# Performance work log

Hardware: AMD Instinct MI355X
Metric: run time of the kernel (lower is better)

Reference implementation:

```python
import jax, jax.numpy as jnp
import numpy as np

ALPHA = 1000.0


def setup_inputs() -> dict:
    key = jax.random.key(0)
    ks = jax.random.split(key, 5)
    B, D_in, K = 8192, 2048, 256  # K = n_clusters = embed_dim (square cluster_reps)
    x = jax.random.normal(ks[0], (B, D_in), dtype=jnp.float32)
    W_enc = jax.random.normal(ks[1], (D_in, K), dtype=jnp.float32) * (1.0 / np.sqrt(D_in))
    b_enc = jnp.zeros((K,), dtype=jnp.float32)
    W_dec = jax.random.normal(ks[2], (K, D_in), dtype=jnp.float32) * (1.0 / np.sqrt(K))
    b_dec = jnp.zeros((D_in,), dtype=jnp.float32)
    cluster_reps = jax.random.normal(ks[3], (K, K), dtype=jnp.float32)
    return {"x": x, "W_enc": W_enc, "b_enc": b_enc, "W_dec": W_dec,
            "b_dec": b_dec, "cluster_reps": cluster_reps}


def reference(x, W_enc, b_enc, W_dec, b_dec, cluster_reps):
    # Autoencoder (linear MLP stand-in for the injected module)
    emb = x @ W_enc + b_enc                    # [B, K]
    reconstruction = emb @ W_dec + b_dec       # [B, D_in]

    # Squared Euclidean distance to each cluster rep, in GEMM form: [B, K]
    # dist[b, k] = ||emb_b||^2 - 2 emb_b . c_k + ||c_k||^2
    dist = (jnp.sum(emb * emb, axis=1, keepdims=True)
            - 2.0 * (emb @ cluster_reps.T)
            + jnp.sum(cluster_reps * cluster_reps, axis=1)[None, :])

    stack_dist = dist.T                        # [K, B] (matches torch.stack over clusters)
    min_dist = jnp.min(stack_dist, axis=0)     # [B]
    stack_exp = jnp.exp(-ALPHA * (stack_dist - min_dist[None, :]))  # stable softmin
    softmax = stack_exp / jnp.sum(stack_exp, axis=0, keepdims=True)
    weighted_dist = stack_dist * softmax       # [K, B]
    return weighted_dist, reconstruction
```

## Files before the change

### kernel.cpp

```cpp
#include <hip/hip_runtime.h>

#define ALPHA_F 1000.0f

typedef _Float16 half8 __attribute__((ext_vector_type(8)));
typedef float floatx4 __attribute__((ext_vector_type(4)));

__device__ __forceinline__ void gload_lds16(const void* g, void* l) {
    __builtin_amdgcn_global_load_lds(
        (const __attribute__((address_space(1))) unsigned int*)g,
        (__attribute__((address_space(3))) unsigned int*)l, 16, 0, 0);
}

__global__ __launch_bounds__(256) void prep(
    const float* __restrict__ W_enc, const float* __restrict__ W_dec,
    const float* __restrict__ creps,
    _Float16* __restrict__ Wh, _Float16* __restrict__ Wl,
    _Float16* __restrict__ Wdh,
    _Float16* __restrict__ Ch, _Float16* __restrict__ Cl,
    float* __restrict__ cnorm)
{
    const int bid = blockIdx.x;
    if (bid < 256) {
        const int q = bid * 256 + threadIdx.x;
        const int n = q & 255, k8 = q >> 8;
        const int k = k8 * 8;
        half8 h, l;
        #pragma unroll
        for (int i = 0; i < 8; ++i) {
            const float v = W_enc[(size_t)(k + i) * 256 + n] * 256.0f;
            const _Float16 hi = (_Float16)v;
            h[i] = hi;
            l[i] = (_Float16)(v - (float)hi);
        }
        const int kc = k >> 5, nt = n >> 4;
        const int lane = (n & 15) | ((k8 & 3) << 4);
        const size_t idx = (size_t)((kc * 16 + nt) * 64 + lane) * 8;
        *(half8*)(Wh + idx) = h;
        *(half8*)(Wl + idx) = l;
    } else if (bid < 512) {
        const int q = (bid - 256) * 256 + threadIdx.x;
        const int n = q & 2047, k8 = q >> 11;
        const int k = k8 * 8;
        half8 h;
        #pragma unroll
        for (int i = 0; i < 8; ++i) h[i] = (_Float16)W_dec[(size_t)(k + i) * 2048 + n];
        const int kc = k8 >> 2, nt = n >> 4;
        const int lane = (n & 15) | ((k8 & 3) << 4);
        *(half8*)(Wdh + (size_t)((kc * 128 + nt) * 64 + lane) * 8) = h;
    } else if (bid < 544) {
        const int q = (bid - 512) * 256 + threadIdx.x;
        const int n = q & 255, j8 = q >> 8;
        const int j = j8 * 8;
        half8 h, l;
        #pragma unroll
        for (int i = 0; i < 8; ++i) {
            const float v = creps[(size_t)n * 256 + j + i];
            const _Float16 hi = (_Float16)v;
            h[i] = hi;
            l[i] = (_Float16)((v - (float)hi) * 2048.0f);
        }
        const int jc = j >> 5, nt = n >> 4;
        const int lane = (n & 15) | ((j8 & 3) << 4);
        const size_t idx = (size_t)((jc * 16 + nt) * 64 + lane) * 8;
        *(half8*)(Ch + idx) = h;
        *(half8*)(Cl + idx) = l;
    } else {
        const int wid = threadIdx.x >> 6, lane = threadIdx.x & 63;
        const int row = (bid - 544) * 4 + wid;
        const float4 v = *(const float4*)(creps + (size_t)row * 256 + lane * 4);
        float s = v.x * v.x + v.y * v.y + v.z * v.z + v.w * v.w;
        #pragma unroll
        for (int off = 32; off >= 1; off >>= 1) s += __shfl_xor(s, off, 64);
        if (lane == 0) cnorm[row] = s;
    }
}

__global__ __launch_bounds__(256) void emb_gemm(
    const float* __restrict__ x, const _Float16* __restrict__ Wh,
    const _Float16* __restrict__ Wl, float* __restrict__ P)
{
    __shared__ _Float16 Ah[2][4 * 64 * 8], Al[2][4 * 64 * 8];
    __shared__ _Float16 Bh[2][16 * 64 * 8], Bl[2][16 * 64 * 8];
    const int t = threadIdx.x, lane = t & 63, w = t >> 6;
    const int kk = blockIdx.x;
    const int mb = blockIdx.y;
    const int m0 = mb * 64;

    const int am = t >> 2, q = t & 3;
    const int aoff = (((am >> 4) * 64) + ((am & 15) | (q << 4))) * 8;
    const float* xP = x + (size_t)(m0 + am) * 2048 + kk * 512 + q * 8;

    floatx4 acc[4][4] = {};

    {
        const float4 v0 = *(const float4*)(xP);
        const float4 v1 = *(const float4*)(xP + 4);
        const int kc = kk * 16;
        const _Float16* bh_src = Wh + (size_t)kc * 16 * 512;
        const _Float16* bl_src = Wl + (size_t)kc * 16 * 512;
        #pragma unroll
        for (int i = 0; i < 4; ++i) {
            const int c = w * 4 + i;
            gload_lds16(bh_src + (size_t)c * 512 + lane * 8, &Bh[0][c * 512]);
            gload_lds16(bl_src + (size_t)c * 512 + lane * 8, &Bl[0][c * 512]);
        }
        const float vv[8] = {v0.x, v0.y, v0.z, v0.w, v1.x, v1.y, v1.z, v1.w};
        half8 h8, l8;
        #pragma unroll
        for (int i = 0; i < 8; ++i) {
            const _Float16 hi = (_Float16)vv[i];
            h8[i] = hi;
            l8[i] = (_Float16)(vv[i] - (float)hi);
        }
        *(half8*)(&Ah[0][aoff]) = h8;
        *(half8*)(&Al[0][aoff]) = l8;
        __syncthreads();
    }

    for (int it = 0; it < 16; ++it) {
        const int buf = it & 1;

        float4 n0, n1;
        if (it < 15) {
            n0 = *(const float4*)(xP + (it + 1) * 32);
            n1 = *(const float4*)(xP + (it + 1) * 32 + 4);
            const int kc = kk * 16 + it + 1;
            const _Float16* bh_src = Wh + (size_t)kc * 16 * 512;
            const _Float16* bl_src = Wl + (size_t)kc * 16 * 512;
            #pragma unroll
            for (int i = 0; i < 4; ++i) {
                const int c = w * 4 + i;
                gload_lds16(bh_src + (size_t)c * 512 + lane * 8, &Bh[buf ^ 1][c * 512]);
                gload_lds16(bl_src + (size_t)c * 512 + lane * 8, &Bl[buf ^ 1][c * 512]);
            }
        }

        half8 ah[4], al[4], bh[4], bl[4];
        #pragma unroll
        for (int s = 0; s < 4; ++s) {
            ah[s] = *(const half8*)(&Ah[buf][(s * 64 + lane) * 8]);
            al[s] = *(const half8*)(&Al[buf][(s * 64 + lane) * 8]);
        }
        #pragma unroll
        for (int ni = 0; ni < 4; ++ni) {
            bh[ni] = *(const half8*)(&Bh[buf][((w * 4 + ni) * 64 + lane) * 8]);
            bl[ni] = *(const half8*)(&Bl[buf][((w * 4 + ni) * 64 + lane) * 8]);
        }
        #pragma unroll
        for (int mi = 0; mi < 4; ++mi) {
            #pragma unroll
            for (int ni = 0; ni < 4; ++ni) {
                acc[mi][ni] = __builtin_amdgcn_mfma_f32_16x16x32_f16(ah[mi], bl[ni], acc[mi][ni], 0, 0, 0);
                acc[mi][ni] = __builtin_amdgcn_mfma_f32_16x16x32_f16(al[mi], bh[ni], acc[mi][ni], 0, 0, 0);
                acc[mi][ni] = __builtin_amdgcn_mfma_f32_16x16x32_f16(ah[mi], bh[ni], acc[mi][ni], 0, 0, 0);
            }
        }

        if (it < 15) {
            const float vv[8] = {n0.x, n0.y, n0.z, n0.w, n1.x, n1.y, n1.z, n1.w};
            half8 h8, l8;
            #pragma unroll
            for (int i = 0; i < 8; ++i) {
                const _Float16 hi = (_Float16)vv[i];
                h8[i] = hi;
                l8[i] = (_Float16)(vv[i] - (float)hi);
            }
            *(half8*)(&Ah[buf ^ 1][aoff]) = h8;
            *(half8*)(&Al[buf ^ 1][aoff]) = l8;
            __syncthreads();
        }
    }

    float* Pk = P + (size_t)kk * 2097152;
    #pragma unroll
    for (int mi = 0; mi < 4; ++mi) {
        #pragma unroll
        for (int ni = 0; ni < 4; ++ni) {
            const int col = w * 64 + ni * 16 + (lane & 15);
            const int rowBase = m0 + mi * 16 + (lane >> 4) * 4;
            #pragma unroll
            for (int r = 0; r < 4; ++r)
                Pk[(size_t)(rowBase + r) * 256 + col] = acc[mi][ni][r];
        }
    }
}

__global__ __launch_bounds__(256) void finalize(
    const float* __restrict__ P, const float* __restrict__ b_enc,
    _Float16* __restrict__ ehg, float* __restrict__ embf,
    float* __restrict__ enorm)
{
    const int t = threadIdx.x;
    const int b0 = blockIdx.x * 32;
    const int row = t >> 3, c8 = t & 7;
    const int grow = b0 + row;

    const float* p0 = P + (size_t)grow * 256 + c8 * 32;
    float4 v[8];
    #pragma unroll
    for (int i = 0; i < 8; ++i) v[i] = *(const float4*)(p0 + i * 4);
    #pragma unroll
    for (int kk = 1; kk < 4; ++kk) {
        const float* pk = p0 + (size_t)kk * 2097152;
        #pragma unroll
        for (int i = 0; i < 8; ++i) {
            const float4 a = *(const float4*)(pk + i * 4);
            v[i].x += a.x; v[i].y += a.y; v[i].z += a.z; v[i].w += a.w;
        }
    }
    const float inv = 1.0f / 256.0f;
    float e[32];
    float ssq = 0.0f;
    #pragma unroll
    for (int i = 0; i < 8; ++i) {
        const float4 b = *(const float4*)(b_enc + c8 * 32 + i * 4);
        e[i * 4 + 0] = v[i].x * inv + b.x;
        e[i * 4 + 1] = v[i].y * inv + b.y;
        e[i * 4 + 2] = v[i].z * inv + b.z;
        e[i * 4 + 3] = v[i].w * inv + b.w;
        ssq += e[i * 4 + 0] * e[i * 4 + 0];
        ssq += e[i * 4 + 1] * e[i * 4 + 1];
        ssq += e[i * 4 + 2] * e[i * 4 + 2];
        ssq += e[i * 4 + 3] * e[i * 4 + 3];
    }
    #pragma unroll
    for (int i = 0; i < 8; ++i) {
        float4 s4;
        s4.x = e[i * 4 + 0]; s4.y = e[i * 4 + 1];
        s4.z = e[i * 4 + 2]; s4.w = e[i * 4 + 3];
        *(float4*)(embf + (size_t)grow * 256 + c8 * 32 + i * 4) = s4;
    }
    #pragma unroll
    for (int oo = 0; oo < 4; ++oo) {
        const int q = c8 * 4 + oo;
        half8 h;
        #pragma unroll
        for (int i = 0; i < 8; ++i) h[i] = (_Float16)e[oo * 8 + i];
        const size_t idx = (size_t)(((grow >> 4) * 8 + (q >> 2)) * 64
                                    + ((grow & 15) | ((q & 3) << 4))) * 8;
        *(half8*)(ehg + idx) = h;
    }
    ssq += __shfl_xor(ssq, 1, 64);
    ssq += __shfl_xor(ssq, 2, 64);
    ssq += __shfl_xor(ssq, 4, 64);
    if (c8 == 0) enorm[grow] = ssq;
}

__global__ __launch_bounds__(256) void dist16(
    const float* __restrict__ embf, const _Float16* __restrict__ ch,
    const _Float16* __restrict__ cl, const float* __restrict__ enorm,
    const float* __restrict__ cnorm, float* __restrict__ out)
{
    __shared__ float D[16 * 257];
    __shared__ float MINV[16], SUMV[16];
    const int t = threadIdx.x, lane = t & 63, w = t >> 6;
    const int b0 = blockIdx.x * 16;
    const int arow16 = lane & 15, aoct = lane >> 4;

    floatx4 acc[4] = {}, accX[4] = {};
    for (int kc = 0; kc < 8; ++kc) {
        const float* fp = embf + (size_t)(b0 + arow16) * 256 + kc * 32 + aoct * 8;
        const float4 u0 = *(const float4*)(fp);
        const float4 u1 = *(const float4*)(fp + 4);
        const float vv[8] = {u0.x, u0.y, u0.z, u0.w, u1.x, u1.y, u1.z, u1.w};
        half8 ah, al;
        #pragma unroll
        for (int j = 0; j < 8; ++j) {
            const _Float16 hi = (_Float16)vv[j];
            ah[j] = hi;
            al[j] = (_Float16)((vv[j] - (float)hi) * 2048.0f);
        }
        #pragma unroll
        for (int ni = 0; ni < 4; ++ni) {
            const size_t bb = (size_t)((kc * 16 + (w * 4 + ni)) * 64 + lane) * 8;
            const half8 bh = *(const half8*)(ch + bb);
            const half8 bl = *(const half8*)(cl + bb);
            acc[ni]  = __builtin_amdgcn_mfma_f32_16x16x32_f16(ah, bh, acc[ni], 0, 0, 0);
            accX[ni] = __builtin_amdgcn_mfma_f32_16x16x32_f16(ah, bl, accX[ni], 0, 0, 0);
            accX[ni] = __builtin_amdgcn_mfma_f32_16x16x32_f16(al, bh, accX[ni], 0, 0, 0);
        }
    }

    const float invs = 1.0f / 2048.0f;
    #pragma unroll
    for (int ni = 0; ni < 4; ++ni) {
        const int k = w * 64 + ni * 16 + (lane & 15);
        const float cn = cnorm[k];
        #pragma unroll
        for (int r = 0; r < 4; ++r) {
            const int rl = (lane >> 4) * 4 + r;
            const float S = acc[ni][r] + accX[ni][r] * invs;
            D[rl * 257 + k] = enorm[b0 + rl] - 2.0f * S + cn;
        }
    }
    __syncthreads();

    #pragma unroll
    for (int rr = 0; rr < 4; ++rr) {
        const int r = w * 4 + rr;
        const float d0 = D[r * 257 + lane +   0];
        const float d1 = D[r * 257 + lane +  64];
        const float d2 = D[r * 257 + lane + 128];
        const float d3 = D[r * 257 + lane + 192];
        float mn = fminf(fminf(d0, d1), fminf(d2, d3));
        #pragma unroll
        for (int off = 32; off >= 1; off >>= 1) mn = fminf(mn, __shfl_xor(mn, off, 64));
        float s = expf(-ALPHA_F * (d0 - mn)) + expf(-ALPHA_F * (d1 - mn))
                + expf(-ALPHA_F * (d2 - mn)) + expf(-ALPHA_F * (d3 - mn));
        #pragma unroll
        for (int off = 32; off >= 1; off >>= 1) s += __shfl_xor(s, off, 64);
        if (lane == 0) { MINV[r] = mn; SUMV[r] = s; }
    }
    __syncthreads();

    const int b = t & 15, kg = t >> 4;
    const float mn = MINV[b], sv = SUMV[b];
    #pragma unroll
    for (int kk = 0; kk < 16; ++kk) {
        const int k = kk * 16 + kg;
        const float dv = D[b * 257 + k];
        out[(size_t)k * 8192 + b0 + b] = dv * expf(-ALPHA_F * (dv - mn)) / sv;
    }
}

__global__ __launch_bounds__(256) void recon_gemm(
    const _Float16* __restrict__ embh, const _Float16* __restrict__ Wdh,
    const float* __restrict__ b_dec, float* __restrict__ out)
{
    __shared__ _Float16 Ah[2][8 * 64 * 8];
    __shared__ _Float16 Bh[2][8 * 64 * 8];
    const int t = threadIdx.x, lane = t & 63, w = t >> 6;
    const int wm = w >> 1, wn = w & 1;
    const int nb = blockIdx.x, mb = blockIdx.y;

    floatx4 acc[4][4] = {};

    #pragma unroll
    for (int i = 0; i < 2; ++i) {
        const int c = w * 2 + i;
        gload_lds16(embh + (size_t)(((mb * 8 + c) * 8 + 0) * 64 + lane) * 8, &Ah[0][c * 512]);
        gload_lds16(Wdh + (size_t)((0 * 128 + nb * 8 + c) * 64 + lane) * 8, &Bh[0][c * 512]);
    }
    __syncthreads();

    for (int kc = 0; kc < 8; ++kc) {
        const int buf = kc & 1;
        if (kc < 7) {
            #pragma unroll
            for (int i = 0; i < 2; ++i) {
                const int c = w * 2 + i;
                gload_lds16(embh + (size_t)(((mb * 8 + c) * 8 + (kc + 1)) * 64 + lane) * 8,
                            &Ah[buf ^ 1][c * 512]);
                gload_lds16(Wdh + (size_t)(((kc + 1) * 128 + nb * 8 + c) * 64 + lane) * 8,
                            &Bh[buf ^ 1][c * 512]);
            }
        }
        half8 a[4], b[4];
        #pragma unroll
        for (int mi = 0; mi < 4; ++mi) a[mi] = *(const half8*)(&Ah[buf][((wm * 4 + mi) * 64 + lane) * 8]);
        #pragma unroll
        for (int ni = 0; ni < 4; ++ni) b[ni] = *(const half8*)(&Bh[buf][((wn * 4 + ni) * 64 + lane) * 8]);
        #pragma unroll
        for (int mi = 0; mi < 4; ++mi)
            #pragma unroll
            for (int ni = 0; ni < 4; ++ni)
                acc[mi][ni] = __builtin_amdgcn_mfma_f32_16x16x32_f16(a[mi], b[ni], acc[mi][ni], 0, 0, 0);
        if (kc < 7) __syncthreads();
    }

    #pragma unroll
    for (int ni = 0; ni < 4; ++ni) {
        const int col = nb * 128 + (wn * 4 + ni) * 16 + (lane & 15);
        const float bias = b_dec[col];
        #pragma unroll
        for (int mi = 0; mi < 4; ++mi) {
            const int rowBase = mb * 128 + (wm * 4 + mi) * 16 + (lane >> 4) * 4;
            #pragma unroll
            for (int r = 0; r < 4; ++r)
                out[(size_t)(rowBase + r) * 2048 + col] = acc[mi][ni][r] + bias;
        }
    }
}

extern "C" void kernel_launch(void* const* d_in, const int* in_sizes, int n_in,
                              void* d_out, int out_size, void* d_ws, size_t ws_size,
                              hipStream_t stream) {
    const float* x     = (const float*)d_in[0];
    const float* W_enc = (const float*)d_in[1];
    const float* b_enc = (const float*)d_in[2];
    const float* W_dec = (const float*)d_in[3];
    const float* b_dec = (const float*)d_in[4];
    const float* creps = (const float*)d_in[5];

    float* out_w   = (float*)d_out;
    float* out_rec = out_w + (size_t)256 * 8192;
    float* P       = out_rec;

    float*     cnorm = (float*)d_ws;
    _Float16*  embh  = (_Float16*)(cnorm + 256);
    _Float16*  Whf   = embh + (size_t)8192 * 256;
    _Float16*  Wlf   = Whf + (size_t)2048 * 256;
    _Float16*  Wdh   = Wlf + (size_t)2048 * 256;
    _Float16*  crh   = Wdh + (size_t)256 * 2048;
    _Float16*  crl   = crh + (size_t)256 * 256;
    float*     enorm = (float*)(crl + (size_t)256 * 256);
    float*     embf  = enorm + 8192;

    prep<<<608, 256, 0, stream>>>(W_enc, W_dec, creps, Whf, Wlf, Wdh, crh, crl, cnorm);

    emb_gemm<<<dim3(4, 128), 256, 0, stream>>>(x, Whf, Wlf, P);

    finalize<<<256, 256, 0, stream>>>(P, b_enc, embh, embf, enorm);

    dist16<<<512, 256, 0, stream>>>(embf, crh, crl, enorm, cnorm, out_w);

    recon_gemm<<<dim3(16, 64), 256, 0, stream>>>(embh, Wdh, b_dec, out_rec);
}
```

Measured before the change: 200.8 us.

## Load GEMM B fragments directly from global into registers instead of LDS

In the embedding GEMM, the W_enc hi/lo B fragments now go straight from global memory into registers. They are double-buffered in registers, and LDS is kept only for the converted x tiles, synchronised with a manual waitcnt and barrier. The reconstruction GEMM drops LDS and barriers entirely and reads A and B fragments directly from global each k-step. The aim is to remove LDS staging traffic and barrier stalls and to cut LDS footprint for occupancy. The cost is more register pressure and redundant global or L2 reads, since fragments are no longer shared through LDS across waves.

```diff
diff --git a/kernel.cpp b/kernel.cpp
--- a/kernel.cpp
+++ b/kernel.cpp
@@ -4,12 +4,6 @@
 
 typedef _Float16 half8 __attribute__((ext_vector_type(8)));
 typedef float floatx4 __attribute__((ext_vector_type(4)));
-
-__device__ __forceinline__ void gload_lds16(const void* g, void* l) {
-    __builtin_amdgcn_global_load_lds(
-        (const __attribute__((address_space(1))) unsigned int*)g,
-        (__attribute__((address_space(3))) unsigned int*)l, 16, 0, 0);
-}
 
 __global__ __launch_bounds__(256) void prep(
     const float* __restrict__ W_enc, const float* __restrict__ W_dec,
@@ -79,8 +73,7 @@
     const float* __restrict__ x, const _Float16* __restrict__ Wh,
     const _Float16* __restrict__ Wl, float* __restrict__ P)
 {
-    __shared__ _Float16 Ah[2][4 * 64 * 8], Al[2][4 * 64 * 8];
-    __shared__ _Float16 Bh[2][16 * 64 * 8], Bl[2][16 * 64 * 8];
+    __shared__ _Float16 Ah[2][2048], Al[2][2048];
     const int t = threadIdx.x, lane = t & 63, w = t >> 6;
     const int kk = blockIdx.x;
     const int mb = blockIdx.y;
@@ -90,20 +83,15 @@
     const int aoff = (((am >> 4) * 64) + ((am & 15) | (q << 4))) * 8;
     const float* xP = x + (size_t)(m0 + am) * 2048 + kk * 512 + q * 8;
 
+    const _Float16* bhP = Wh + (size_t)((kk * 256 + w * 4) * 64 + lane) * 8;
+    const _Float16* blP = Wl + (size_t)((kk * 256 + w * 4) * 64 + lane) * 8;
+
     floatx4 acc[4][4] = {};
+    half8 bh[4], bl[4];
 
     {
         const float4 v0 = *(const float4*)(xP);
         const float4 v1 = *(const float4*)(xP + 4);
-        const int kc = kk * 16;
-        const _Float16* bh_src = Wh + (size_t)kc * 16 * 512;
-        const _Float16* bl_src = Wl + (size_t)kc * 16 * 512;
-        #pragma unroll
-        for (int i = 0; i < 4; ++i) {
-            const int c = w * 4 + i;
-            gload_lds16(bh_src + (size_t)c * 512 + lane * 8, &Bh[0][c * 512]);
-            gload_lds16(bl_src + (size_t)c * 512 + lane * 8, &Bl[0][c * 512]);
-        }
         const float vv[8] = {v0.x, v0.y, v0.z, v0.w, v1.x, v1.y, v1.z, v1.w};
         half8 h8, l8;
         #pragma unroll
@@ -114,38 +102,39 @@
         }
         *(half8*)(&Ah[0][aoff]) = h8;
         *(half8*)(&Al[0][aoff]) = l8;
-        __syncthreads();
-    }
-
+        #pragma unroll
+        for (int ni = 0; ni < 4; ++ni) {
+            bh[ni] = *(const half8*)(bhP + ni * 512);
+            bl[ni] = *(const half8*)(blP + ni * 512);
+        }
+        asm volatile("s_waitcnt lgkmcnt(0)" ::: "memory");
+        __builtin_amdgcn_sched_barrier(0);
+        __builtin_amdgcn_s_barrier();
+    }
+
+    #pragma unroll 2
     for (int it = 0; it < 16; ++it) {
         const int buf = it & 1;
 
         float4 n0, n1;
+        half8 nbh[4], nbl[4];
         if (it < 15) {
             n0 = *(const float4*)(xP + (it + 1) * 32);
             n1 = *(const float4*)(xP + (it + 1) * 32 + 4);
-            const int kc = kk * 16 + it + 1;
-            const _Float16* bh_src = Wh + (size_t)kc * 16 * 512;
-            const _Float16* bl_src = Wl + (size_t)kc * 16 * 512;
-            #pragma unroll
-            for (int i = 0; i < 4; ++i) {
-                const int c = w * 4 + i;
-                gload_lds16(bh_src + (size_t)c * 512 + lane * 8, &Bh[buf ^ 1][c * 512]);
-                gload_lds16(bl_src + (size_t)c * 512 + lane * 8, &Bl[buf ^ 1][c * 512]);
+            #pragma unroll
+            for (int ni = 0; ni < 4; ++ni) {
+                nbh[ni] = *(const half8*)(bhP + (size_t)(it + 1) * 8192 + ni * 512);
+                nbl[ni] = *(const half8*)(blP + (size_t)(it + 1) * 8192 + ni * 512);
             }
         }
 
-        half8 ah[4], al[4], bh[4], bl[4];
+        half8 ah[4], al[4];
         #pragma unroll
         for (int s = 0; s < 4; ++s) {
             ah[s] = *(const half8*)(&Ah[buf][(s * 64 + lane) * 8]);
             al[s] = *(const half8*)(&Al[buf][(s * 64 + lane) * 8]);
         }
-        #pragma unroll
-        for (int ni = 0; ni < 4; ++ni) {
-            bh[ni] = *(const half8*)(&Bh[buf][((w * 4 + ni) * 64 + lane) * 8]);
-            bl[ni] = *(const half8*)(&Bl[buf][((w * 4 + ni) * 64 + lane) * 8]);
-        }
+
         #pragma unroll
         for (int mi = 0; mi < 4; ++mi) {
             #pragma unroll
@@ -167,7 +156,11 @@
             }
             *(half8*)(&Ah[buf ^ 1][aoff]) = h8;
             *(half8*)(&Al[buf ^ 1][aoff]) = l8;
-            __syncthreads();
+            #pragma unroll
+            for (int ni = 0; ni < 4; ++ni) { bh[ni] = nbh[ni]; bl[ni] = nbl[ni]; }
+            asm volatile("s_waitcnt lgkmcnt(0)" ::: "memory");
+            __builtin_amdgcn_sched_barrier(0);
+            __builtin_amdgcn_s_barrier();
         }
     }
 
@@ -327,8 +320,6 @@
     const _Float16* __restrict__ embh, const _Float16* __restrict__ Wdh,
     const float* __restrict__ b_dec, float* __restrict__ out)
 {
-    __shared__ _Float16 Ah[2][8 * 64 * 8];
-    __shared__ _Float16 Bh[2][8 * 64 * 8];
     const int t = threadIdx.x, lane = t & 63, w = t >> 6;
     const int wm = w >> 1, wn = w & 1;
     const int nb = blockIdx.x, mb = blockIdx.y;
@@ -336,36 +327,19 @@
     floatx4 acc[4][4] = {};
 
     #pragma unroll
-    for (int i = 0; i < 2; ++i) {
-        const int c = w * 2 + i;
-        gload_lds16(embh + (size_t)(((mb * 8 + c) * 8 + 0) * 64 + lane) * 8, &Ah[0][c * 512]);
-        gload_lds16(Wdh + (size_t)((0 * 128 + nb * 8 + c) * 64 + lane) * 8, &Bh[0][c * 512]);
-    }
-    __syncthreads();
-
     for (int kc = 0; kc < 8; ++kc) {
-        const int buf = kc & 1;
-        if (kc < 7) {
-            #pragma unroll
-            for (int i = 0; i < 2; ++i) {
-                const int c = w * 2 + i;
-                gload_lds16(embh + (size_t)(((mb * 8 + c) * 8 + (kc + 1)) * 64 + lane) * 8,
-                            &Ah[buf ^ 1][c * 512]);
-                gload_lds16(Wdh + (size_t)(((kc + 1) * 128 + nb * 8 + c) * 64 + lane) * 8,
-                            &Bh[buf ^ 1][c * 512]);
-            }
-        }
         half8 a[4], b[4];
         #pragma unroll
-        for (int mi = 0; mi < 4; ++mi) a[mi] = *(const half8*)(&Ah[buf][((wm * 4 + mi) * 64 + lane) * 8]);
-        #pragma unroll
-        for (int ni = 0; ni < 4; ++ni) b[ni] = *(const half8*)(&Bh[buf][((wn * 4 + ni) * 64 + lane) * 8]);
+        for (int mi = 0; mi < 4; ++mi)
+            a[mi] = *(const half8*)(embh + (size_t)(((mb * 8 + wm * 4 + mi) * 8 + kc) * 64 + lane) * 8);
+        #pragma unroll
+        for (int ni = 0; ni < 4; ++ni)
+            b[ni] = *(const half8*)(Wdh + (size_t)((kc * 128 + nb * 8 + wn * 4 + ni) * 64 + lane) * 8);
         #pragma unroll
         for (int mi = 0; mi < 4; ++mi)
             #pragma unroll
             for (int ni = 0; ni < 4; ++ni)
                 acc[mi][ni] = __builtin_amdgcn_mfma_f32_16x16x32_f16(a[mi], b[ni], acc[mi][ni], 0, 0, 0);
-        if (kc < 7) __syncthreads();
     }
 
     #pragma unroll
```

Result: faster. 195.9 us (-2.4%).
